# Kernel tuning notes

Hardware: AMD Instinct MI355X
Metric: run time of the kernel (lower is better)

The kernel has to match this reference:

```python
import jax, jax.numpy as jnp
import numpy as np

N_NODES = 100000
N_EDGES = 3200000
F_IN = 512
HIDDEN = 16
N_CLASS = 10


def gcn_conv(x, edge_index, W, b):
    """PyG-style GCNConv: sym-normalized aggregation with self-loops.
    out = D^{-1/2} (A + I) D^{-1/2} X W + b
    """
    n = x.shape[0]
    loop = jnp.arange(n, dtype=edge_index.dtype)
    src = jnp.concatenate([edge_index[0], loop])  # [E+N]
    dst = jnp.concatenate([edge_index[1], loop])  # [E+N]
    # degree of target nodes (includes self-loops, so deg >= 1)
    deg = jax.ops.segment_sum(jnp.ones_like(src, dtype=x.dtype), dst, num_segments=n)
    dinv = jax.lax.rsqrt(deg)  # safe: deg >= 1
    norm = dinv[src] * dinv[dst]  # [E+N]
    h = x @ W  # [N, out] — transform before gather (cheaper when out < in)
    msg = h[src] * norm[:, None]  # gather + scale
    out = jax.ops.segment_sum(msg, dst, num_segments=n)  # scatter-add
    return out + b


def setup_inputs() -> dict:
    key = jax.random.key(0)
    k1, k2, k3, k4, k5, k6 = jax.random.split(key, 6)
    x = jax.random.normal(k1, (N_NODES, F_IN), dtype=jnp.float32)
    edge_index = jax.random.randint(k2, (2, N_EDGES), 0, N_NODES, dtype=jnp.int64)
    s1 = 1.0 / np.sqrt(F_IN)
    s2 = 1.0 / np.sqrt(HIDDEN)
    W1 = jax.random.uniform(k3, (F_IN, HIDDEN), jnp.float32, -s1, s1)
    b1 = jax.random.uniform(k4, (HIDDEN,), jnp.float32, -s1, s1)
    W2 = jax.random.uniform(k5, (HIDDEN, N_CLASS), jnp.float32, -s2, s2)
    b2 = jax.random.uniform(k6, (N_CLASS,), jnp.float32, -s2, s2)
    return {"x": x, "edge_index": edge_index, "W1": W1, "b1": b1, "W2": W2, "b2": b2}


def reference(x, edge_index, W1, b1, W2, b2):
    h = gcn_conv(x, edge_index, W1, b1)
    h = jax.nn.relu(h)
    # Dropout(p=0.5) is identity in eval/inference mode
    out = gcn_conv(h, edge_index, W2, b2)
    return out
```

## Files before the change

### kernel.cpp

```cpp
#include <hip/hip_runtime.h>

#define N_NODES 100000
#define N_EDGES 3200000
#define F_IN    512
#define HIDDEN  16
#define N_CLASS 10

#define NBUCK   196
#define BSH     9
#define EPB     4096
#define NPART   ((N_EDGES + EPB - 1) / EPB)
#define PCAP    18432

__device__ __forceinline__ int load_idx(const void* ei, int is32, long long pos) {
    return is32 ? ((const int*)ei)[pos] : (int)((const long long*)ei)[pos];
}

__global__ void k_init(const unsigned* __restrict__ ei, int* __restrict__ bsize,
                       int* __restrict__ det) {
    int t = threadIdx.x;
    if (t < NBUCK) bsize[t] = 0;
    if (t == 0) det[0] = 0;
    __syncthreads();
    unsigned odd = 0;
    for (int i = t; i < 4096; i += 256) odd |= ei[2 * i + 1];
    if (odd) atomicOr(&det[0], 1);
}

__global__ __launch_bounds__(256) void k_bhist(const void* __restrict__ ei,
                                               const int* __restrict__ det,
                                               int* __restrict__ bsize) {
    __shared__ int hist[NBUCK];
    int t = threadIdx.x;
    long long e0 = (long long)blockIdx.x * EPB;
    long long e1 = e0 + EPB; if (e1 > N_EDGES) e1 = N_EDGES;
    int is32 = det[0];
    if (t < NBUCK) hist[t] = 0;
    __syncthreads();
    for (long long e = e0 + t; e < e1; e += 256) {
        int d = load_idx(ei, is32, N_EDGES + e);
        atomicAdd(&hist[d >> BSH], 1);
    }
    __syncthreads();
    if (t < NBUCK && hist[t]) atomicAdd(&bsize[t], hist[t]);
}

__global__ void k_bucketscan(const int* __restrict__ bsize, int* __restrict__ bbase,
                             int* __restrict__ bcur) {
    __shared__ int s[256];
    int t = threadIdx.x;
    int v = (t < NBUCK) ? bsize[t] : 0;
    s[t] = v;
    __syncthreads();
    for (int off = 1; off < 256; off <<= 1) {
        int u = (t >= off) ? s[t - off] : 0;
        __syncthreads();
        s[t] += u;
        __syncthreads();
    }
    if (t < NBUCK) { int ex = s[t] - v; bbase[t] = ex; bcur[t] = ex; }
}

__global__ __launch_bounds__(256) void k_part(const void* __restrict__ ei,
                                              const int* __restrict__ det,
                                              int* __restrict__ bcur,
                                              unsigned* __restrict__ buf) {
    __shared__ int hist[NBUCK];
    __shared__ int base[NBUCK];
    __shared__ int lcur[NBUCK];
    int t = threadIdx.x;
    long long e0 = (long long)blockIdx.x * EPB;
    long long e1 = e0 + EPB; if (e1 > N_EDGES) e1 = N_EDGES;
    int is32 = det[0];
    if (t < NBUCK) { hist[t] = 0; lcur[t] = 0; }
    __syncthreads();
    for (long long e = e0 + t; e < e1; e += 256) {
        int d = load_idx(ei, is32, N_EDGES + e);
        atomicAdd(&hist[d >> BSH], 1);
    }
    __syncthreads();
    if (t < NBUCK) base[t] = hist[t] ? atomicAdd(&bcur[t], hist[t]) : 0;
    __syncthreads();
    for (long long e = e0 + t; e < e1; e += 256) {
        int s = load_idx(ei, is32, e);
        int d = load_idx(ei, is32, (long long)N_EDGES + e);
        int b = d >> BSH;
        int off = atomicAdd(&lcur[b], 1);
        buf[base[b] + off] = ((unsigned)s << BSH) | (unsigned)(d & 511);
    }
}

__global__ __launch_bounds__(256) void k_degscan(const unsigned* __restrict__ buf,
                                                 const int* __restrict__ bbase,
                                                 const int* __restrict__ bsize,
                                                 int* __restrict__ rowptr,
                                                 float* __restrict__ dinv) {
    __shared__ int s[512];
    int t = threadIdx.x;
    int b = blockIdx.x;
    s[t] = 0; s[t + 256] = 0;
    __syncthreads();
    int j0 = bbase[b], j1 = j0 + bsize[b];
    for (int j = j0 + t; j < j1; j += 256)
        atomicAdd(&s[buf[j] & 511], 1);
    __syncthreads();
    int o0 = s[t], o1 = s[t + 256];
    for (int off = 1; off < 512; off <<= 1) {
        int v0 = (t >= off) ? s[t - off] : 0;
        int v1 = s[t + 256 - off];
        __syncthreads();
        s[t] += v0; s[t + 256] += v1;
        __syncthreads();
    }
    int nb0 = b << BSH;
    int base = bbase[b];
    int n0 = nb0 + t, n1 = nb0 + t + 256;
    if (n0 < N_NODES) { rowptr[n0] = base + s[t] - o0;       dinv[n0] = rsqrtf((float)(o0 + 1)); }
    if (n1 < N_NODES) { rowptr[n1] = base + s[t + 256] - o1; dinv[n1] = rsqrtf((float)(o1 + 1)); }
    if (b == NBUCK - 1 && t == 0) rowptr[N_NODES] = N_EDGES;
}

__global__ __launch_bounds__(256) void k_place3(const unsigned* __restrict__ buf,
                                                const int* __restrict__ bbase,
                                                const int* __restrict__ bsize,
                                                const int* __restrict__ rowptr,
                                                int* __restrict__ csr) {
    __shared__ int lptr[512];
    __shared__ int outb[PCAP];
    int t = threadIdx.x;
    int b = blockIdx.x;
    int jb = bbase[b];
    int sz = bsize[b];
    int nb0 = b << BSH;
    int csrbase = rowptr[nb0];
    for (int i = t; i < 512; i += 256) {
        int n = nb0 + i;
        lptr[i] = (n < N_NODES) ? rowptr[n] - csrbase : sz;
    }
    __syncthreads();
    for (int j = t; j < sz; j += 256) {
        unsigned p = buf[jb + j];
        int pos = atomicAdd(&lptr[p & 511], 1);
        int s = (int)(p >> BSH);
        if (pos < PCAP) outb[pos] = s;
        else            csr[csrbase + pos] = s;
    }
    __syncthreads();
    int lim = sz < PCAP ? sz : PCAP;
    for (int j = t; j < lim; j += 256) csr[csrbase + j] = outb[j];
}

__global__ __launch_bounds__(256) void k_gemv1(const float* __restrict__ x,
                                               const float* __restrict__ W1,
                                               const float* __restrict__ dinv,
                                               float* __restrict__ hs) {
    __shared__ float red[3][64][17];
    int t = threadIdx.x;
    int r = t & 63;
    int seg = t >> 6;
    int n = blockIdx.x * 64 + r;
    bool valid = n < N_NODES;
    const float4* xr = (const float4*)(x + (valid ? (size_t)n * F_IN : 0) + seg * 128);
    float acc[16];
#pragma unroll
    for (int k = 0; k < 16; ++k) acc[k] = 0.f;
    float4 cur0 = xr[0], cur1 = xr[1], cur2 = xr[2], cur3 = xr[3];
#pragma unroll 1
    for (int ch = 0; ch < 8; ++ch) {
        float4 nx0, nx1, nx2, nx3;
        if (ch < 7) {
            nx0 = xr[(ch + 1) * 4 + 0]; nx1 = xr[(ch + 1) * 4 + 1];
            nx2 = xr[(ch + 1) * 4 + 2]; nx3 = xr[(ch + 1) * 4 + 3];
        }
        const float* wp = W1 + (seg * 128 + ch * 16) * HIDDEN;
#pragma unroll
        for (int k = 0; k < 16; ++k)
            acc[k] += cur0.x * wp[0 * 16 + k] + cur0.y * wp[1 * 16 + k]
                    + cur0.z * wp[2 * 16 + k] + cur0.w * wp[3 * 16 + k];
#pragma unroll
        for (int k = 0; k < 16; ++k)
            acc[k] += cur1.x * wp[4 * 16 + k] + cur1.y * wp[5 * 16 + k]
                    + cur1.z * wp[6 * 16 + k] + cur1.w * wp[7 * 16 + k];
#pragma unroll
        for (int k = 0; k < 16; ++k)
            acc[k] += cur2.x * wp[8 * 16 + k] + cur2.y * wp[9 * 16 + k]
                    + cur2.z * wp[10 * 16 + k] + cur2.w * wp[11 * 16 + k];
#pragma unroll
        for (int k = 0; k < 16; ++k)
            acc[k] += cur3.x * wp[12 * 16 + k] + cur3.y * wp[13 * 16 + k]
                    + cur3.z * wp[14 * 16 + k] + cur3.w * wp[15 * 16 + k];
        if (ch < 7) { cur0 = nx0; cur1 = nx1; cur2 = nx2; cur3 = nx3; }
    }
    if (seg) {
#pragma unroll
        for (int k = 0; k < 16; ++k) red[seg - 1][r][k] = acc[k];
    }
    __syncthreads();
    if (seg == 0 && valid) {
#pragma unroll
        for (int k = 0; k < 16; ++k)
            acc[k] += red[0][r][k] + red[1][r][k] + red[2][r][k];
        float di = dinv[n];
        float4* o = (float4*)&hs[(size_t)n * HIDDEN];
        o[0] = make_float4(acc[0] * di,  acc[1] * di,  acc[2] * di,  acc[3] * di);
        o[1] = make_float4(acc[4] * di,  acc[5] * di,  acc[6] * di,  acc[7] * di);
        o[2] = make_float4(acc[8] * di,  acc[9] * di,  acc[10] * di, acc[11] * di);
        o[3] = make_float4(acc[12] * di, acc[13] * di, acc[14] * di, acc[15] * di);
    }
}

__global__ __launch_bounds__(256) void k_agg1(const int* __restrict__ rowptr,
                                              const int* __restrict__ csr,
                                              const float* __restrict__ hs,
                                              const float* __restrict__ dinv,
                                              const float* __restrict__ b1,
                                              const float* __restrict__ W2,
                                              float* __restrict__ ts) {
    __shared__ float sh[16][17];
    int t  = threadIdx.x;
    int ln = t >> 4;
    int k  = t & 15;
    int n  = blockIdx.x * 16 + ln;
    bool valid = n < N_NODES;
    int r0 = valid ? rowptr[n] : 0;
    int r1 = valid ? rowptr[n + 1] : 0;
    float acc = valid ? hs[(size_t)n * HIDDEN + k] : 0.f;
    int j = r0;
    for (; j + 8 <= r1; j += 8) {
        int s0 = csr[j],     s1 = csr[j + 1], s2 = csr[j + 2], s3 = csr[j + 3];
        int s4 = csr[j + 4], s5 = csr[j + 5], s6 = csr[j + 6], s7 = csr[j + 7];
        float v0 = hs[(size_t)s0 * HIDDEN + k];
        float v1 = hs[(size_t)s1 * HIDDEN + k];
        float v2 = hs[(size_t)s2 * HIDDEN + k];
        float v3 = hs[(size_t)s3 * HIDDEN + k];
        float v4 = hs[(size_t)s4 * HIDDEN + k];
        float v5 = hs[(size_t)s5 * HIDDEN + k];
        float v6 = hs[(size_t)s6 * HIDDEN + k];
        float v7 = hs[(size_t)s7 * HIDDEN + k];
        acc += ((v0 + v1) + (v2 + v3)) + ((v4 + v5) + (v6 + v7));
    }
    for (; j + 4 <= r1; j += 4) {
        int s0 = csr[j], s1 = csr[j + 1], s2 = csr[j + 2], s3 = csr[j + 3];
        float v0 = hs[(size_t)s0 * HIDDEN + k];
        float v1 = hs[(size_t)s1 * HIDDEN + k];
        float v2 = hs[(size_t)s2 * HIDDEN + k];
        float v3 = hs[(size_t)s3 * HIDDEN + k];
        acc += (v0 + v1) + (v2 + v3);
    }
    for (; j < r1; ++j) acc += hs[(size_t)csr[j] * HIDDEN + k];
    float di = valid ? dinv[n] : 0.f;
    float h = di * acc + b1[k];
    sh[ln][k] = h > 0.f ? h : 0.f;
    __syncthreads();
    int c = (k < N_CLASS) ? k : 0;
    float o = 0.f;
#pragma unroll
    for (int kk = 0; kk < HIDDEN; ++kk) o += sh[ln][kk] * W2[kk * N_CLASS + c];
    if (valid) ts[(size_t)n * 16 + k] = (k < N_CLASS) ? o * di : 0.f;
}

__global__ __launch_bounds__(256) void k_agg2(const int* __restrict__ rowptr,
                                              const int* __restrict__ csr,
                                              const float* __restrict__ ts,
                                              const float* __restrict__ dinv,
                                              const float* __restrict__ b2,
                                              float* __restrict__ out) {
    int t  = threadIdx.x;
    int ln = t >> 4;
    int c  = t & 15;
    int n  = blockIdx.x * 16 + ln;
    if (n >= N_NODES) return;
    int r0 = rowptr[n], r1 = rowptr[n + 1];
    float acc = ts[(size_t)n * 16 + c];
    int j = r0;
    for (; j + 8 <= r1; j += 8) {
        int s0 = csr[j],     s1 = csr[j + 1], s2 = csr[j + 2], s3 = csr[j + 3];
        int s4 = csr[j + 4], s5 = csr[j + 5], s6 = csr[j + 6], s7 = csr[j + 7];
        float v0 = ts[(size_t)s0 * 16 + c];
        float v1 = ts[(size_t)s1 * 16 + c];
        float v2 = ts[(size_t)s2 * 16 + c];
        float v3 = ts[(size_t)s3 * 16 + c];
        float v4 = ts[(size_t)s4 * 16 + c];
        float v5 = ts[(size_t)s5 * 16 + c];
        float v6 = ts[(size_t)s6 * 16 + c];
        float v7 = ts[(size_t)s7 * 16 + c];
        acc += ((v0 + v1) + (v2 + v3)) + ((v4 + v5) + (v6 + v7));
    }
    for (; j + 4 <= r1; j += 4) {
        int s0 = csr[j], s1 = csr[j + 1], s2 = csr[j + 2], s3 = csr[j + 3];
        float v0 = ts[(size_t)s0 * 16 + c];
        float v1 = ts[(size_t)s1 * 16 + c];
        float v2 = ts[(size_t)s2 * 16 + c];
        float v3 = ts[(size_t)s3 * 16 + c];
        acc += (v0 + v1) + (v2 + v3);
    }
    for (; j < r1; ++j) acc += ts[(size_t)csr[j] * 16 + c];
    if (c < N_CLASS) out[(size_t)n * N_CLASS + c] = dinv[n] * acc + b2[c];
}

extern "C" void kernel_launch(void* const* d_in, const int* in_sizes, int n_in,
                              void* d_out, int out_size, void* d_ws, size_t ws_size,
                              hipStream_t stream) {
    const float* x  = (const float*)d_in[0];
    const void*  ei = d_in[1];
    const float* W1 = (const float*)d_in[2];
    const float* b1 = (const float*)d_in[3];
    const float* W2 = (const float*)d_in[4];
    const float* b2 = (const float*)d_in[5];
    float* out = (float*)d_out;
    float* ws  = (float*)d_ws;

    float* dinv   = ws;
    int*   rowptr = (int*)(ws + 100096);
    int*   bsize  = (int*)(ws + 200512);
    int*   bbase  = (int*)(ws + 200768);
    int*   bcur   = (int*)(ws + 201024);
    int*   det    = (int*)(ws + 201280);
    int*   csr    = (int*)(ws + 201344);
    float* hs     = ws + 3401344;
    float* ts     = ws + 5001344;
    unsigned* buf = (unsigned*)(ws + 3401344);

    k_init      <<<1, 256, 0, stream>>>((const unsigned*)ei, bsize, det);
    k_bhist     <<<NPART, 256, 0, stream>>>(ei, det, bsize);
    k_bucketscan<<<1, 256, 0, stream>>>(bsize, bbase, bcur);
    k_part      <<<NPART, 256, 0, stream>>>(ei, det, bcur, buf);
    k_degscan   <<<NBUCK, 256, 0, stream>>>(buf, bbase, bsize, rowptr, dinv);
    k_place3    <<<NBUCK, 256, 0, stream>>>(buf, bbase, bsize, rowptr, csr);

    k_gemv1<<<(N_NODES + 63) / 64, 256, 0, stream>>>(x, W1, dinv, hs);

    k_agg1<<<(N_NODES + 15) / 16, 256, 0, stream>>>(rowptr, csr, hs, dinv, b1, W2, ts);
    k_agg2<<<(N_NODES + 15) / 16, 256, 0, stream>>>(rowptr, csr, ts, dinv, b2, out);
}
```

Measured before the change: 585.6 us.

## Stage X tiles in shared memory and split hidden outputs across wavefronts

Replaces the per-row GEMV, where each thread streamed a strided quarter of its row and partial sums were reduced through LDS, with a tiled kernel. Coalesced 64x64 tiles of X are staged through padded shared memory, with the next chunk prefetched into registers. Each wavefront computes 4 of the 16 hidden outputs from a transposed copy of W1 that a new small kernel produces. This aims to coalesce the dominant 200MB read of X and cut register pressure, at the cost of two barriers per chunk and an extra launch.

```diff
diff --git a/kernel.cpp b/kernel.cpp
--- a/kernel.cpp
+++ b/kernel.cpp
@@ -5,6 +5,10 @@
 #define F_IN    512
 #define HIDDEN  16
 #define N_CLASS 10
+
+#define TILE_R  64
+#define KC      64
+#define XSTRIDE 68
 
 #define NBUCK   196
 #define BSH     9
@@ -150,62 +154,70 @@
     for (int j = t; j < lim; j += 256) csr[csrbase + j] = outb[j];
 }
 
-__global__ __launch_bounds__(256) void k_gemv1(const float* __restrict__ x,
-                                               const float* __restrict__ W1,
+__global__ void k_wt(const float* __restrict__ W1, float* __restrict__ Wt) {
+    int t = blockIdx.x * 256 + threadIdx.x;
+    if (t < F_IN * HIDDEN) {
+        int k = t >> 9;
+        int j = t & (F_IN - 1);
+        Wt[t] = W1[j * HIDDEN + k];
+    }
+}
+
+__global__ __launch_bounds__(256) void k_gemm1(const float* __restrict__ x,
+                                               const float* __restrict__ Wt,
                                                const float* __restrict__ dinv,
                                                float* __restrict__ hs) {
-    __shared__ float red[3][64][17];
-    int t = threadIdx.x;
-    int r = t & 63;
-    int seg = t >> 6;
-    int n = blockIdx.x * 64 + r;
-    bool valid = n < N_NODES;
-    const float4* xr = (const float4*)(x + (valid ? (size_t)n * F_IN : 0) + seg * 128);
-    float acc[16];
-#pragma unroll
-    for (int k = 0; k < 16; ++k) acc[k] = 0.f;
-    float4 cur0 = xr[0], cur1 = xr[1], cur2 = xr[2], cur3 = xr[3];
+    __shared__ float sX[TILE_R * XSTRIDE];
+    int t = threadIdx.x;
+    int lane = t & 63;
+    int rowbase = blockIdx.x * TILE_R;
+    int kbase = __builtin_amdgcn_readfirstlane((t >> 6) << 2);
+    const float* wk = Wt + kbase * F_IN;
+
+    float4 r[4];
+#pragma unroll
+    for (int i = 0; i < 4; ++i) {
+        int f = i * 256 + t, row = f >> 4, c4 = f & 15;
+        int grow = rowbase + row;
+        r[i] = make_float4(0.f, 0.f, 0.f, 0.f);
+        if (grow < N_NODES)
+            r[i] = ((const float4*)(x + (size_t)grow * F_IN))[c4];
+    }
+    float acc[4] = {};
 #pragma unroll 1
-    for (int ch = 0; ch < 8; ++ch) {
-        float4 nx0, nx1, nx2, nx3;
-        if (ch < 7) {
-            nx0 = xr[(ch + 1) * 4 + 0]; nx1 = xr[(ch + 1) * 4 + 1];
-            nx2 = xr[(ch + 1) * 4 + 2]; nx3 = xr[(ch + 1) * 4 + 3];
+    for (int ch = 0; ch < F_IN / KC; ++ch) {
+#pragma unroll
+        for (int i = 0; i < 4; ++i) {
+            int f = i * 256 + t, row = f >> 4, c4 = f & 15;
+            *((float4*)&sX[row * XSTRIDE + c4 * 4]) = r[i];
         }
-        const float* wp = W1 + (seg * 128 + ch * 16) * HIDDEN;
-#pragma unroll
-        for (int k = 0; k < 16; ++k)
-            acc[k] += cur0.x * wp[0 * 16 + k] + cur0.y * wp[1 * 16 + k]
-                    + cur0.z * wp[2 * 16 + k] + cur0.w * wp[3 * 16 + k];
-#pragma unroll
-        for (int k = 0; k < 16; ++k)
-            acc[k] += cur1.x * wp[4 * 16 + k] + cur1.y * wp[5 * 16 + k]
-                    + cur1.z * wp[6 * 16 + k] + cur1.w * wp[7 * 16 + k];
-#pragma unroll
-        for (int k = 0; k < 16; ++k)
-            acc[k] += cur2.x * wp[8 * 16 + k] + cur2.y * wp[9 * 16 + k]
-                    + cur2.z * wp[10 * 16 + k] + cur2.w * wp[11 * 16 + k];
-#pragma unroll
-        for (int k = 0; k < 16; ++k)
-            acc[k] += cur3.x * wp[12 * 16 + k] + cur3.y * wp[13 * 16 + k]
-                    + cur3.z * wp[14 * 16 + k] + cur3.w * wp[15 * 16 + k];
-        if (ch < 7) { cur0 = nx0; cur1 = nx1; cur2 = nx2; cur3 = nx3; }
-    }
-    if (seg) {
-#pragma unroll
-        for (int k = 0; k < 16; ++k) red[seg - 1][r][k] = acc[k];
-    }
-    __syncthreads();
-    if (seg == 0 && valid) {
-#pragma unroll
-        for (int k = 0; k < 16; ++k)
-            acc[k] += red[0][r][k] + red[1][r][k] + red[2][r][k];
-        float di = dinv[n];
-        float4* o = (float4*)&hs[(size_t)n * HIDDEN];
-        o[0] = make_float4(acc[0] * di,  acc[1] * di,  acc[2] * di,  acc[3] * di);
-        o[1] = make_float4(acc[4] * di,  acc[5] * di,  acc[6] * di,  acc[7] * di);
-        o[2] = make_float4(acc[8] * di,  acc[9] * di,  acc[10] * di, acc[11] * di);
-        o[3] = make_float4(acc[12] * di, acc[13] * di, acc[14] * di, acc[15] * di);
+        __syncthreads();
+        if (ch + 1 < F_IN / KC) {
+#pragma unroll
+            for (int i = 0; i < 4; ++i) {
+                int f = i * 256 + t, row = f >> 4, c4 = f & 15;
+                int grow = rowbase + row;
+                r[i] = make_float4(0.f, 0.f, 0.f, 0.f);
+                if (grow < N_NODES)
+                    r[i] = ((const float4*)(x + (size_t)grow * F_IN + (ch + 1) * KC))[c4];
+            }
+        }
+#pragma unroll
+        for (int js = 0; js < KC; js += 4) {
+            float4 xv = *((const float4*)&sX[lane * XSTRIDE + js]);
+#pragma unroll
+            for (int kk = 0; kk < 4; ++kk) {
+                const float* wp = wk + kk * F_IN + ch * KC + js;
+                acc[kk] += xv.x * wp[0] + xv.y * wp[1] + xv.z * wp[2] + xv.w * wp[3];
+            }
+        }
+        __syncthreads();
+    }
+    int grow = rowbase + lane;
+    if (grow < N_NODES) {
+        float di = dinv[grow];
+        *((float4*)&hs[(size_t)grow * HIDDEN + kbase]) =
+            make_float4(acc[0] * di, acc[1] * di, acc[2] * di, acc[3] * di);
     }
 }
 
@@ -319,6 +331,7 @@
     int*   csr    = (int*)(ws + 201344);
     float* hs     = ws + 3401344;
     float* ts     = ws + 5001344;
+    float* Wt     = ws + 6601344;
     unsigned* buf = (unsigned*)(ws + 3401344);
 
     k_init      <<<1, 256, 0, stream>>>((const unsigned*)ei, bsize, det);
@@ -328,7 +341,8 @@
     k_degscan   <<<NBUCK, 256, 0, stream>>>(buf, bbase, bsize, rowptr, dinv);
     k_place3    <<<NBUCK, 256, 0, stream>>>(buf, bbase, bsize, rowptr, csr);
 
-    k_gemv1<<<(N_NODES + 63) / 64, 256, 0, stream>>>(x, W1, dinv, hs);
+    k_wt   <<<(F_IN * HIDDEN) / 256, 256, 0, stream>>>(W1, Wt);
+    k_gemm1<<<(N_NODES + TILE_R - 1) / TILE_R, 256, 0, stream>>>(x, Wt, dinv, hs);
 
     k_agg1<<<(N_NODES + 15) / 16, 256, 0, stream>>>(rowptr, csr, hs, dinv, b1, W2, ts);
     k_agg2<<<(N_NODES + 15) / 16, 256, 0, stream>>>(rowptr, csr, ts, dinv, b2, out);
```

New measurement: 521.7 us. -10.9%, faster.
